# Kernel optimization log

Hardware: AMD Instinct MI355X
Metric: run time of the kernel (lower is better)

## Reference

```python
import jax, jax.numpy as jnp
import numpy as np

# dims: batch, fast time, fast/slow embed, heads, rate, ffn hidden, pool hidden, recombine hidden
B, T, D = 2, 2048, 512
H = 8
R = 8
DS = 512
FF = 2048
HP = 2048
HR = 2048


def _ln(x, g, b):
    m = jnp.mean(x, axis=-1, keepdims=True)
    v = jnp.var(x, axis=-1, keepdims=True)
    return (x - m) / jnp.sqrt(v + 1e-5) * g + b


def _encoder_layer(x, ln1_g, ln1_b, wqkv, bqkv, wo, bo, ln2_g, ln2_b, w1, b1, w2, b2, n_heads):
    # pre-LN transformer encoder layer with causal self-attention
    b_, t, d = x.shape
    dh = d // n_heads
    h = _ln(x, ln1_g, ln1_b)
    qkv = h @ wqkv + bqkv  # [B,T,3D]
    q, k, v = jnp.split(qkv, 3, axis=-1)
    q = q.reshape(b_, t, n_heads, dh)
    k = k.reshape(b_, t, n_heads, dh)
    v = v.reshape(b_, t, n_heads, dh)
    scores = jnp.einsum('bqhd,bkhd->bhqk', q, k) / jnp.sqrt(jnp.float32(dh))
    mask = jnp.tril(jnp.ones((t, t), dtype=bool))
    scores = jnp.where(mask, scores, jnp.finfo(scores.dtype).min)
    a = jax.nn.softmax(scores, axis=-1)
    o = jnp.einsum('bhqk,bkhd->bqhd', a, v).reshape(b_, t, d)
    x = x + o @ wo + bo
    h2 = _ln(x, ln2_g, ln2_b)
    return x + jax.nn.gelu(h2 @ w1 + b1) @ w2 + b2


def _pool(f, rate, wp1, bp1, wp2, bp2):
    # causal pooling: s_k = FFN(f_{k*rate : (k+1)*rate}), prepend zero step, drop last
    b_, t, d = f.shape
    k = t // rate
    xb = f[:, :k * rate].reshape(b_, k, rate * d)  # [B,K,rate*D] block flatten
    s = jax.nn.gelu(xb @ wp1 + bp1) @ wp2 + bp2  # [B,K,DS]
    s0 = jnp.zeros((b_, 1, s.shape[-1]), s.dtype)
    return jnp.concatenate([s0, s[:, :-1]], axis=1)


def _recombine(zf, zs, rate, wr1, br1, wr2, br2):
    # lift slow to fast scale (repeat_interleave along time), concat channels, 2-layer MLP
    zl = jnp.repeat(zs, rate, axis=1)[:, :zf.shape[1]]
    x = jnp.concatenate([zf, zl], axis=-1)
    return jax.nn.gelu(x @ wr1 + br1) @ wr2 + br2


def setup_inputs() -> dict:
    key = jax.random.key(0)
    ks = iter(jax.random.split(key, 64))

    def w(shape):
        return jax.random.normal(next(ks), shape, dtype=jnp.float32) * 0.02

    def z(shape):
        return jnp.zeros(shape, dtype=jnp.float32)

    def o(shape):
        return jnp.ones(shape, dtype=jnp.float32)

    inp = {'x': jax.random.normal(next(ks), (B, T, D), dtype=jnp.float32)}
    for suf, dm, ff in (('f', D, FF), ('s', DS, FF)):
        inp['ln1' + suf + '_g'] = o((dm,)); inp['ln1' + suf + '_b'] = z((dm,))
        inp['wqkv_' + suf] = w((dm, 3 * dm)); inp['bqkv_' + suf] = z((3 * dm,))
        inp['wo_' + suf] = w((dm, dm)); inp['bo_' + suf] = z((dm,))
        inp['ln2' + suf + '_g'] = o((dm,)); inp['ln2' + suf + '_b'] = z((dm,))
        inp['w1_' + suf] = w((dm, ff)); inp['b1_' + suf] = z((ff,))
        inp['w2_' + suf] = w((ff, dm)); inp['b2_' + suf] = z((dm,))
    inp['wp1'] = w((R * D, HP)); inp['bp1'] = z((HP,))
    inp['wp2'] = w((HP, DS)); inp['bp2'] = z((DS,))
    inp['wr1'] = w((D + DS, HR)); inp['br1'] = z((HR,))
    inp['wr2'] = w((HR, D)); inp['br2'] = z((D,))
    return inp


def reference(x, ln1f_g, ln1f_b, wqkv_f, bqkv_f, wo_f, bo_f, ln2f_g, ln2f_b, w1_f, b1_f, w2_f, b2_f,
              ln1s_g, ln1s_b, wqkv_s, bqkv_s, wo_s, bo_s, ln2s_g, ln2s_b, w1_s, b1_s, w2_s, b2_s,
              wp1, bp1, wp2, bp2, wr1, br1, wr2, br2):
    # fast-scale encoder layer
    zf = _encoder_layer(x, ln1f_g, ln1f_b, wqkv_f, bqkv_f, wo_f, bo_f,
                        ln2f_g, ln2f_b, w1_f, b1_f, w2_f, b2_f, H)
    # causal pool fast -> slow
    zs_in = _pool(zf, R, wp1, bp1, wp2, bp2)
    # slow-scale encoder layer
    zs = _encoder_layer(zs_in, ln1s_g, ln1s_b, wqkv_s, bqkv_s, wo_s, bo_s,
                        ln2s_g, ln2s_b, w1_s, b1_s, w2_s, b2_s, H)
    # lift + recombine back to fast scale
    return _recombine(zf, zs, R, wr1, br1, wr2, br2)
```

## Files before the change

kernel.cpp:

```cpp
#include <hip/hip_runtime.h>
#include <cstdint>

#define DEV __device__ __forceinline__

typedef float  floatx4 __attribute__((ext_vector_type(4)));
typedef __bf16 bf16x8  __attribute__((ext_vector_type(8)));
typedef short  short8  __attribute__((ext_vector_type(8)));

DEV unsigned short f2bf(float f) {
  unsigned u = __builtin_bit_cast(unsigned, f);
  u += 0x7FFFu + ((u >> 16) & 1u);
  return (unsigned short)(u >> 16);
}
DEV float bf2f(unsigned short s) {
  unsigned u = ((unsigned)s) << 16;
  return __builtin_bit_cast(float, u);
}
DEV float gelu_f(float x) {
  float x3 = x * x * x;
  return 0.5f * x * (1.0f + tanhf(0.7978845608028654f * (x + 0.044715f * x3)));
}

DEV void stage16(const unsigned short* g, unsigned short* l) {
  __builtin_amdgcn_global_load_lds(
      (const __attribute__((address_space(1))) void*)g,
      (__attribute__((address_space(3))) void*)l, 16, 0, 0);
}

struct TrArgs {
  const float* src[12];
  unsigned short* dst[12];
  int K[12];
  int N[12];
  int off[13];
};

__global__ __launch_bounds__(256) void transpose_all_k(TrArgs a) {
  __shared__ unsigned short tile[32][33];
  int bid = blockIdx.x;
  int w = 0;
#pragma unroll
  for (int i = 0; i < 11; ++i) if (bid >= a.off[i + 1]) w = i + 1;
  int loc = bid - a.off[w];
  int tn = a.N[w] >> 5;
  int nt = (loc % tn) * 32, kt = (loc / tn) * 32;
  const float* W = a.src[w];
  unsigned short* WT = a.dst[w];
  int K = a.K[w], N = a.N[w];

  int t = threadIdx.x;
  int rr = t >> 3, c4 = (t & 7) * 4;
  const float* src = W + (size_t)(kt + rr) * N + nt + c4;
  float4 v = *reinterpret_cast<const float4*>(src);
  tile[rr][c4 + 0] = f2bf(v.x); tile[rr][c4 + 1] = f2bf(v.y);
  tile[rr][c4 + 2] = f2bf(v.z); tile[rr][c4 + 3] = f2bf(v.w);
  __syncthreads();
  unsigned short* dst = WT + (size_t)(nt + rr) * K + kt + c4;
  ushort4 o;
  o.x = tile[c4 + 0][rr]; o.y = tile[c4 + 1][rr];
  o.z = tile[c4 + 2][rr]; o.w = tile[c4 + 3][rr];
  *reinterpret_cast<ushort4*>(dst) = o;
}

template <int NP, int ACT, int RES, int OBF>
__global__ __launch_bounds__(256) void reduceN_k(const float* __restrict__ part,
                                                 const float* __restrict__ bias,
                                                 const float* __restrict__ resid,
                                                 void* __restrict__ out,
                                                 int MN, int Nmask) {
  int i = (blockIdx.x * 256 + threadIdx.x) * 4;
  if (i >= MN) return;
  float4 v = *reinterpret_cast<const float4*>(&part[i]);
#pragma unroll
  for (int p = 1; p < NP; ++p) {
    float4 t = *reinterpret_cast<const float4*>(&part[(size_t)p * MN + i]);
    v.x += t.x; v.y += t.y; v.z += t.z; v.w += t.w;
  }
  float4 bv = *reinterpret_cast<const float4*>(&bias[i & Nmask]);
  v.x += bv.x; v.y += bv.y; v.z += bv.z; v.w += bv.w;
  if (RES) {
    float4 r = *reinterpret_cast<const float4*>(&resid[i]);
    v.x += r.x; v.y += r.y; v.z += r.z; v.w += r.w;
  }
  if (ACT) { v.x = gelu_f(v.x); v.y = gelu_f(v.y); v.z = gelu_f(v.z); v.w = gelu_f(v.w); }
  if (OBF) {
    ushort4 o; o.x = f2bf(v.x); o.y = f2bf(v.y); o.z = f2bf(v.z); o.w = f2bf(v.w);
    *reinterpret_cast<ushort4*>(&((unsigned short*)out)[i]) = o;
  } else {
    *reinterpret_cast<float4*>(&((float*)out)[i]) = v;
  }
}

__global__ __launch_bounds__(64) void ln_k(const float* __restrict__ in,
                                           const float* __restrict__ g,
                                           const float* __restrict__ be,
                                           unsigned short* __restrict__ out) {
  int row = blockIdx.x, lane = threadIdx.x;
  const float* p = in + (size_t)row * 512;
  float v[8], s = 0.f, sq = 0.f;
#pragma unroll
  for (int j = 0; j < 8; ++j) { v[j] = p[j * 64 + lane]; s += v[j]; sq += v[j] * v[j]; }
#pragma unroll
  for (int off = 32; off; off >>= 1) { s += __shfl_xor(s, off, 64); sq += __shfl_xor(sq, off, 64); }
  float mean = s * (1.f / 512.f);
  float var  = sq * (1.f / 512.f) - mean * mean;
  float rstd = rsqrtf(var + 1e-5f);
#pragma unroll
  for (int j = 0; j < 8; ++j) {
    int c = j * 64 + lane;
    out[(size_t)row * 512 + c] = f2bf((v[j] - mean) * rstd * g[c] + be[c]);
  }
}

__global__ __launch_bounds__(64) void rsln_k(const float* __restrict__ part,
                                             const float* __restrict__ bias,
                                             const float* __restrict__ g,
                                             const float* __restrict__ be,
                                             float* __restrict__ zsin,
                                             unsigned short* __restrict__ sh) {
  const int MN = 512 * 512;
  int j = blockIdx.x, lane = threadIdx.x;
  int k = j & 255;
  float v[8], s = 0.f, sq = 0.f;
  if (k == 0) {
#pragma unroll
    for (int jj = 0; jj < 8; ++jj) { v[jj] = 0.f; zsin[(size_t)j * 512 + jj * 64 + lane] = 0.f; }
  } else {
    const float* p = part + (size_t)(j - 1) * 512;
#pragma unroll
    for (int jj = 0; jj < 8; ++jj) {
      int c = jj * 64 + lane;
      float t = bias[c];
#pragma unroll
      for (int pp = 0; pp < 4; ++pp) t += p[(size_t)pp * MN + c];
      v[jj] = t;
      zsin[(size_t)j * 512 + c] = t;
      s += t; sq += t * t;
    }
  }
#pragma unroll
  for (int off = 32; off; off >>= 1) { s += __shfl_xor(s, off, 64); sq += __shfl_xor(sq, off, 64); }
  float mean = s * (1.f / 512.f);
  float var  = sq * (1.f / 512.f) - mean * mean;
  float rstd = rsqrtf(var + 1e-5f);
#pragma unroll
  for (int jj = 0; jj < 8; ++jj) {
    int c = jj * 64 + lane;
    sh[(size_t)j * 512 + c] = f2bf((v[jj] - mean) * rstd * g[c] + be[c]);
  }
}

template <int TM, int TN, int ACT, int RES, int OBF, int SPLITK, int CAT = 0>
__global__ __launch_bounds__(256) void gemm_k(const unsigned short* __restrict__ A,
                                              const unsigned short* __restrict__ A2,
                                              const unsigned short* __restrict__ WT,
                                              const float* __restrict__ bias,
                                              const float* __restrict__ resid,
                                              void* __restrict__ out,
                                              int M, int K, int N) {
  constexpr int WMn = (TN == 64) ? 2 : (TM / 64);
  constexpr int WNn = 4 / WMn;
  constexpr int MI  = TM / WMn / 16;
  constexpr int SN  = TN / WNn / 16;
  constexpr int APW = TM / 32;
  constexpr int BPW = TN / 32;
  __shared__ __align__(16) unsigned short As[2][TM * 64];
  __shared__ __align__(16) unsigned short Bs[2][TN * 64];
  const int tid  = threadIdx.x;
  const int wv = tid >> 6, lane = tid & 63;
  const int wm = wv / WNn, wn = wv % WNn;
  const int quad = lane >> 4, l16 = lane & 15;
  const int m0 = blockIdx.y * TM, n0 = blockIdx.x * TN;
  const int sp = (SPLITK > 1) ? blockIdx.z : 0;
  const int Kc = K / SPLITK;
  const int kb0 = sp * Kc;
  const int nk = Kc / 64;
  const int lrow = lane >> 3;
  const int scol = ((lane & 7) ^ lrow) * 8;
  const int sx = l16 & 7;

  floatx4 acc[MI][SN] = {};

  auto stage = [&](int buf, int kb) {
#pragma unroll
    for (int u = 0; u < APW; ++u) {
      int g = wv * APW + u;
      if (CAT) {
        int row = m0 + g * 8 + lrow;
        int kc = kb + scol;
        const unsigned short* s1 = A + (size_t)row * 512 + kc;
        const unsigned short* s2 = A2 +
            ((size_t)((row >> 11) * 256 + ((row & 2047) >> 3))) * 512 + (kc - 512);
        stage16(kc < 512 ? s1 : s2, &As[buf][g * 512]);
      } else {
        stage16(A + (size_t)(m0 + g * 8 + lrow) * K + kb + scol, &As[buf][g * 512]);
      }
    }
#pragma unroll
    for (int u = 0; u < BPW; ++u) {
      int g = wv * BPW + u;
      stage16(WT + (size_t)(n0 + g * 8 + lrow) * K + kb + scol, &Bs[buf][g * 512]);
    }
  };

  stage(0, kb0);
  __syncthreads();

  for (int t = 0; t < nk; ++t) {
    const int buf = t & 1;
    if (t + 1 < nk) stage(buf ^ 1, kb0 + (t + 1) * 64);
    bf16x8 af[MI][2], bfr[SN][2];
#pragma unroll
    for (int i = 0; i < MI; ++i) {
      const int r = wm * (MI * 16) + i * 16 + l16;
#pragma unroll
      for (int kk = 0; kk < 2; ++kk)
        af[i][kk] = *reinterpret_cast<const bf16x8*>(
            &As[buf][r * 64 + (((kk * 4 + quad) ^ sx) * 8)]);
    }
#pragma unroll
    for (int j = 0; j < SN; ++j) {
      const int r = wn * (SN * 16) + j * 16 + l16;
#pragma unroll
      for (int kk = 0; kk < 2; ++kk)
        bfr[j][kk] = *reinterpret_cast<const bf16x8*>(
            &Bs[buf][r * 64 + (((kk * 4 + quad) ^ sx) * 8)]);
    }
#pragma unroll
    for (int i = 0; i < MI; ++i)
#pragma unroll
      for (int j = 0; j < SN; ++j) {
        acc[i][j] = __builtin_amdgcn_mfma_f32_16x16x32_bf16(af[i][0], bfr[j][0], acc[i][j], 0, 0, 0);
        acc[i][j] = __builtin_amdgcn_mfma_f32_16x16x32_bf16(af[i][1], bfr[j][1], acc[i][j], 0, 0, 0);
      }
    __syncthreads();
  }

#pragma unroll
  for (int i = 0; i < MI; ++i) {
    int row_base = m0 + wm * (MI * 16) + i * 16 + quad * 4;
#pragma unroll
    for (int j = 0; j < SN; ++j) {
      int col = n0 + wn * (SN * 16) + j * 16 + l16;
      float bv = (SPLITK > 1) ? 0.f : bias[col];
#pragma unroll
      for (int rr = 0; rr < 4; ++rr) {
        int row = row_base + rr;
        float v = acc[i][j][rr];
        if (SPLITK > 1) {
          ((float*)out)[((size_t)sp * M + row) * N + col] = v;
        } else {
          v += bv;
          if (RES) v += resid[(size_t)row * N + col];
          if (ACT) v = gelu_f(v);
          if (OBF) ((unsigned short*)out)[(size_t)row * N + col] = f2bf(v);
          else     ((float*)out)[(size_t)row * N + col] = v;
        }
      }
    }
  }
}

__global__ __launch_bounds__(256) void attn_k(const unsigned short* __restrict__ qkv,
                                              unsigned short* __restrict__ out, int T) {
  const int ld = 1536, Dm = 512;
  __shared__ unsigned short Ks[2][64 * 72];
  __shared__ unsigned short Vt[2][64 * 72];
  __shared__ unsigned short ps[4][16 * 72];
  const int tid = threadIdx.x, wv = tid >> 6, lane = tid & 63;
  const int quad = lane >> 4, l16 = lane & 15;
  const int nqt = T >> 6;
  const int z = blockIdx.x;
  const int bh = z & 15;
  const int qt = nqt - 1 - (z >> 4);
  const int b = bh >> 3, hh = bh & 7;
  const int q0 = qt * 64 + wv * 16;
  const size_t bT = (size_t)b * T;

  const unsigned short* qp = qkv + (bT + q0 + l16) * ld + hh * 64 + quad * 8;
  short8 qa = *reinterpret_cast<const short8*>(qp);
  short8 qb = *reinterpret_cast<const short8*>(qp + 32);
  unsigned short qs0[8] __attribute__((aligned(16)));
  unsigned short qs1[8] __attribute__((aligned(16)));
#pragma unroll
  for (int u = 0; u < 8; ++u) {
    qs0[u] = f2bf(bf2f((unsigned short)qa[u]) * 0.125f);
    qs1[u] = f2bf(bf2f((unsigned short)qb[u]) * 0.125f);
  }
  bf16x8 aq0 = *reinterpret_cast<const bf16x8*>(qs0);
  bf16x8 aq1 = *reinterpret_cast<const bf16x8*>(qs1);

  floatx4 O[4] = {};
  float l_r[4] = {0.f, 0.f, 0.f, 0.f};

  const int nch = qt + 1;
  const int skey = tid >> 2, scc = (tid & 3) * 16;
  const int vkey = (tid & 31) * 2, vdg = tid >> 5;

  short8 kA, kB, vA, vB;
  auto prefetch = [&](int c) {
    const unsigned short* kp = qkv + (bT + c * 64 + skey) * ld + Dm + hh * 64 + scc;
    kA = *reinterpret_cast<const short8*>(kp);
    kB = *reinterpret_cast<const short8*>(kp + 8);
    const unsigned short* vp = qkv + (bT + c * 64 + vkey) * ld + 1024 + hh * 64 + vdg * 8;
    vA = *reinterpret_cast<const short8*>(vp);
    vB = *reinterpret_cast<const short8*>(vp + ld);
  };
  auto stage = [&](int buf) {
    *reinterpret_cast<short8*>(&Ks[buf][skey * 72 + scc])     = kA;
    *reinterpret_cast<short8*>(&Ks[buf][skey * 72 + scc + 8]) = kB;
#pragma unroll
    for (int u = 0; u < 8; ++u) {
      unsigned pk = ((unsigned)(unsigned short)vB[u] << 16) | (unsigned short)vA[u];
      *reinterpret_cast<unsigned*>(&Vt[buf][(vdg * 8 + u) * 72 + vkey]) = pk;
    }
  };

  prefetch(0);
  stage(0);
  __syncthreads();

  for (int c = 0; c < nch; ++c) {
    const int buf = c & 1;
    const bool last = (c == nch - 1);
    if (!last) prefetch(c + 1);

    floatx4 S[4];
    __builtin_amdgcn_s_setprio(1);
#pragma unroll
    for (int sub = 0; sub < 4; ++sub) {
      const unsigned short* kr = &Ks[buf][(sub * 16 + l16) * 72 + quad * 8];
      bf16x8 b0 = *reinterpret_cast<const bf16x8*>(kr);
      bf16x8 b1 = *reinterpret_cast<const bf16x8*>(kr + 32);
      floatx4 sacc = {};
      sacc = __builtin_amdgcn_mfma_f32_16x16x32_bf16(aq0, b0, sacc, 0, 0, 0);
      sacc = __builtin_amdgcn_mfma_f32_16x16x32_bf16(aq1, b1, sacc, 0, 0, 0);
      S[sub] = sacc;
    }
    __builtin_amdgcn_s_setprio(0);

    if (last) {
      const int k0 = c * 64;
#pragma unroll
      for (int r = 0; r < 4; ++r) {
        int qg = q0 + quad * 4 + r;
#pragma unroll
        for (int sub = 0; sub < 4; ++sub) {
          int kg = k0 + sub * 16 + l16;
          if (kg > qg) S[sub][r] = -3.0e38f;
        }
      }
    }
#pragma unroll
    for (int sub = 0; sub < 4; ++sub)
#pragma unroll
      for (int r = 0; r < 4; ++r) {
        float p = __expf(S[sub][r]);
        S[sub][r] = p;
        l_r[r] += p;
      }

#pragma unroll
    for (int sub = 0; sub < 4; ++sub)
#pragma unroll
      for (int r = 0; r < 4; ++r)
        ps[wv][(quad * 4 + r) * 72 + sub * 16 + l16] = f2bf(S[sub][r]);
    bf16x8 p0 = *reinterpret_cast<const bf16x8*>(&ps[wv][l16 * 72 + quad * 8]);
    bf16x8 p1 = *reinterpret_cast<const bf16x8*>(&ps[wv][l16 * 72 + 32 + quad * 8]);

    __builtin_amdgcn_s_setprio(1);
#pragma unroll
    for (int sd = 0; sd < 4; ++sd) {
      const unsigned short* vr = &Vt[buf][(sd * 16 + l16) * 72 + quad * 8];
      bf16x8 v0 = *reinterpret_cast<const bf16x8*>(vr);
      bf16x8 v1 = *reinterpret_cast<const bf16x8*>(vr + 32);
      O[sd] = __builtin_amdgcn_mfma_f32_16x16x32_bf16(p0, v0, O[sd], 0, 0, 0);
      O[sd] = __builtin_amdgcn_mfma_f32_16x16x32_bf16(p1, v1, O[sd], 0, 0, 0);
    }
    __builtin_amdgcn_s_setprio(0);

    if (!last) stage((c + 1) & 1);
    __syncthreads();
  }

#pragma unroll
  for (int r = 0; r < 4; ++r) {
    float l = l_r[r];
    l += __shfl_xor(l, 1, 64);
    l += __shfl_xor(l, 2, 64);
    l += __shfl_xor(l, 4, 64);
    l += __shfl_xor(l, 8, 64);
    l_r[r] = l;
  }

#pragma unroll
  for (int sd = 0; sd < 4; ++sd)
#pragma unroll
    for (int r = 0; r < 4; ++r) {
      int qg = q0 + quad * 4 + r;
      out[(bT + qg) * Dm + hh * 64 + sd * 16 + l16] = f2bf(O[sd][r] / l_r[r]);
    }
}

extern "C" void kernel_launch(void* const* d_in, const int* in_sizes, int n_in,
                              void* d_out, int out_size, void* d_ws, size_t ws_size,
                              hipStream_t stream) {
  (void)in_sizes; (void)n_in; (void)out_size; (void)ws_size;
  const int B = 2, T = 2048, FF = 2048, HP = 2048, HR = 2048;
  const int BT = B * T;
  const int BK = B * 256;

  const float* x      = (const float*)d_in[0];
  const float* ln1f_g = (const float*)d_in[1];
  const float* ln1f_b = (const float*)d_in[2];
  const float* wqkv_f = (const float*)d_in[3];
  const float* bqkv_f = (const float*)d_in[4];
  const float* wo_f   = (const float*)d_in[5];
  const float* bo_f   = (const float*)d_in[6];
  const float* ln2f_g = (const float*)d_in[7];
  const float* ln2f_b = (const float*)d_in[8];
  const float* w1_f   = (const float*)d_in[9];
  const float* b1_f   = (const float*)d_in[10];
  const float* w2_f   = (const float*)d_in[11];
  const float* b2_f   = (const float*)d_in[12];
  const float* ln1s_g = (const float*)d_in[13];
  const float* ln1s_b = (const float*)d_in[14];
  const float* wqkv_s = (const float*)d_in[15];
  const float* bqkv_s = (const float*)d_in[16];
  const float* wo_s   = (const float*)d_in[17];
  const float* bo_s   = (const float*)d_in[18];
  const float* ln2s_g = (const float*)d_in[19];
  const float* ln2s_b = (const float*)d_in[20];
  const float* w1_s   = (const float*)d_in[21];
  const float* b1_s   = (const float*)d_in[22];
  const float* w2_s   = (const float*)d_in[23];
  const float* b2_s   = (const float*)d_in[24];
  const float* wp1    = (const float*)d_in[25];
  const float* bp1    = (const float*)d_in[26];
  const float* wp2    = (const float*)d_in[27];
  const float* bp2    = (const float*)d_in[28];
  const float* wr1    = (const float*)d_in[29];
  const float* br1    = (const float*)d_in[30];
  const float* wr2    = (const float*)d_in[31];
  const float* br2    = (const float*)d_in[32];

  char* ws = (char*)d_ws;
  const size_t HMB = 512 * 1024;
  unsigned short* wtbase = (unsigned short*)(ws);
  unsigned short* h      = (unsigned short*)(ws + 76  * HMB);
  unsigned short* qkv    = (unsigned short*)(ws + 84  * HMB);
  unsigned short* attn   = (unsigned short*)(ws + 108 * HMB);
  float*          x1     = (float*)(ws + 116 * HMB);
  unsigned short* mid    = (unsigned short*)(ws + 132 * HMB);
  unsigned short* zf     = (unsigned short*)(ws + 164 * HMB);
  unsigned short* pmid   = (unsigned short*)(ws + 84  * HMB);
  float*          zsin   = (float*)(ws + 90  * HMB);
  unsigned short* sh     = (unsigned short*)(ws + 92  * HMB);
  unsigned short* sqkv   = (unsigned short*)(ws + 93  * HMB);
  unsigned short* sattn  = (unsigned short*)(ws + 96  * HMB);
  float*          sx1    = (float*)(ws + 97  * HMB);
  unsigned short* smid   = (unsigned short*)(ws + 99  * HMB);
  unsigned short* szs    = (unsigned short*)(ws + 103 * HMB);
  float*          part   = (float*)(ws + 172 * HMB);
  unsigned short* mid2   = (unsigned short*)(ws + 240 * HMB);

  size_t wo_off = 0;
  auto walloc = [&](size_t n) { unsigned short* p = wtbase + wo_off; wo_off += n; return p; };
  unsigned short* t_qkv_f = walloc((size_t)512 * 1536);
  unsigned short* t_wo_f  = walloc((size_t)512 * 512);
  unsigned short* t_w1_f  = walloc((size_t)512 * 2048);
  unsigned short* t_w2_f  = walloc((size_t)2048 * 512);
  unsigned short* t_qkv_s = walloc((size_t)512 * 1536);
  unsigned short* t_wo_s  = walloc((size_t)512 * 512);
  unsigned short* t_w1_s  = walloc((size_t)512 * 2048);
  unsigned short* t_w2_s  = walloc((size_t)2048 * 512);
  unsigned short* t_wp1   = walloc((size_t)4096 * 2048);
  unsigned short* t_wp2   = walloc((size_t)2048 * 512);
  unsigned short* t_wr1   = walloc((size_t)1024 * 2048);
  unsigned short* t_wr2   = walloc((size_t)2048 * 512);

  {
    TrArgs a;
    const float* srcs[12] = {wqkv_f, wo_f, w1_f, w2_f, wqkv_s, wo_s, w1_s, w2_s,
                             wp1, wp2, wr1, wr2};
    unsigned short* dsts[12] = {t_qkv_f, t_wo_f, t_w1_f, t_w2_f, t_qkv_s, t_wo_s,
                                t_w1_s, t_w2_s, t_wp1, t_wp2, t_wr1, t_wr2};
    int Ks[12] = {512, 512, 512, 2048, 512, 512, 512, 2048, 4096, 2048, 1024, 2048};
    int Ns[12] = {1536, 512, 2048, 512, 1536, 512, 2048, 512, 2048, 512, 2048, 512};
    int off = 0;
    for (int i = 0; i < 12; ++i) {
      a.src[i] = srcs[i]; a.dst[i] = dsts[i]; a.K[i] = Ks[i]; a.N[i] = Ns[i];
      a.off[i] = off;
      off += (Ks[i] / 32) * (Ns[i] / 32);
    }
    a.off[12] = off;
    transpose_all_k<<<off, 256, 0, stream>>>(a);
  }

  ln_k<<<BT, 64, 0, stream>>>(x, ln1f_g, ln1f_b, h);
  gemm_k<64, 128, 0, 0, 1, 1><<<dim3(12, 64), 256, 0, stream>>>(h, nullptr, t_qkv_f, bqkv_f, nullptr, qkv, BT, 512, 1536);
  attn_k<<<(T / 64) * 16, 256, 0, stream>>>(qkv, attn, T);
  gemm_k<64, 64, 0, 1, 0, 1><<<dim3(8, 64), 256, 0, stream>>>(attn, nullptr, t_wo_f, bo_f, x, x1, BT, 512, 512);
  ln_k<<<BT, 64, 0, stream>>>(x1, ln2f_g, ln2f_b, h);
  gemm_k<128, 128, 1, 0, 1, 1><<<dim3(16, 32), 256, 0, stream>>>(h, nullptr, t_w1_f, b1_f, nullptr, mid, BT, 512, FF);
  gemm_k<64, 64, 0, 1, 1, 1><<<dim3(8, 64), 256, 0, stream>>>(mid, nullptr, t_w2_f, b2_f, x1, zf, BT, FF, 512);

  gemm_k<128, 128, 0, 0, 0, 4><<<dim3(16, 4, 4), 256, 0, stream>>>(zf, nullptr, t_wp1, nullptr, nullptr, part, BK, 4096, HP);
  reduceN_k<4, 1, 0, 1><<<(BK * HP) / 1024, 256, 0, stream>>>(part, bp1, nullptr, pmid, BK * HP, HP - 1);
  gemm_k<64, 64, 0, 0, 0, 4><<<dim3(8, 8, 4), 256, 0, stream>>>(pmid, nullptr, t_wp2, nullptr, nullptr, part, BK, HP, 512);
  rsln_k<<<BK, 64, 0, stream>>>(part, bp2, ln1s_g, ln1s_b, zsin, sh);

  gemm_k<64, 64, 0, 0, 1, 1><<<dim3(24, 8), 256, 0, stream>>>(sh, nullptr, t_qkv_s, bqkv_s, nullptr, sqkv, BK, 512, 1536);
  attn_k<<<(256 / 64) * 16, 256, 0, stream>>>(sqkv, sattn, 256);
  gemm_k<64, 64, 0, 1, 0, 1><<<dim3(8, 8), 256, 0, stream>>>(sattn, nullptr, t_wo_s, bo_s, zsin, sx1, BK, 512, 512);
  ln_k<<<BK, 64, 0, stream>>>(sx1, ln2s_g, ln2s_b, sh);
  gemm_k<64, 64, 1, 0, 1, 1><<<dim3(32, 8), 256, 0, stream>>>(sh, nullptr, t_w1_s, b1_s, nullptr, smid, BK, 512, FF);
  gemm_k<64, 64, 0, 1, 1, 1><<<dim3(8, 8), 256, 0, stream>>>(smid, nullptr, t_w2_s, b2_s, sx1, szs, BK, FF, 512);

  gemm_k<128, 128, 1, 0, 1, 1, 1><<<dim3(16, 32), 256, 0, stream>>>(zf, szs, t_wr1, br1, nullptr, mid2, BT, 1024, HR);
  gemm_k<64, 64, 0, 0, 0, 1><<<dim3(8, 64), 256, 0, stream>>>(mid2, nullptr, t_wr2, br2, nullptr, d_out, BT, HR, 512);
}
```

Before: 429.8 us.

## Compute transposed attention scores to keep P in registers and load K directly

```diff
diff --git a/kernel.cpp b/kernel.cpp
--- a/kernel.cpp
+++ b/kernel.cpp
@@ -264,9 +264,7 @@
 __global__ __launch_bounds__(256) void attn_k(const unsigned short* __restrict__ qkv,
                                               unsigned short* __restrict__ out, int T) {
   const int ld = 1536, Dm = 512;
-  __shared__ unsigned short Ks[2][64 * 72];
   __shared__ unsigned short Vt[2][64 * 72];
-  __shared__ unsigned short ps[4][16 * 72];
   const int tid = threadIdx.x, wv = tid >> 6, lane = tid & 63;
   const int quad = lane >> 4, l16 = lane & 15;
   const int nqt = T >> 6;
@@ -291,24 +289,27 @@
   bf16x8 aq1 = *reinterpret_cast<const bf16x8*>(qs1);
 
   floatx4 O[4] = {};
-  float l_r[4] = {0.f, 0.f, 0.f, 0.f};
+  float l_sum = 0.f;
 
   const int nch = qt + 1;
-  const int skey = tid >> 2, scc = (tid & 3) * 16;
   const int vkey = (tid & 31) * 2, vdg = tid >> 5;
 
-  short8 kA, kB, vA, vB;
-  auto prefetch = [&](int c) {
-    const unsigned short* kp = qkv + (bT + c * 64 + skey) * ld + Dm + hh * 64 + scc;
-    kA = *reinterpret_cast<const short8*>(kp);
-    kB = *reinterpret_cast<const short8*>(kp + 8);
+  short8 kf[4][2];
+  auto loadK = [&](int c) {
+#pragma unroll
+    for (int sub = 0; sub < 4; ++sub) {
+      const unsigned short* kp = qkv + (bT + c * 64 + sub * 16 + l16) * ld + Dm + hh * 64 + quad * 8;
+      kf[sub][0] = *reinterpret_cast<const short8*>(kp);
+      kf[sub][1] = *reinterpret_cast<const short8*>(kp + 32);
+    }
+  };
+  short8 vA, vB;
+  auto prefetchV = [&](int c) {
     const unsigned short* vp = qkv + (bT + c * 64 + vkey) * ld + 1024 + hh * 64 + vdg * 8;
     vA = *reinterpret_cast<const short8*>(vp);
     vB = *reinterpret_cast<const short8*>(vp + ld);
   };
-  auto stage = [&](int buf) {
-    *reinterpret_cast<short8*>(&Ks[buf][skey * 72 + scc])     = kA;
-    *reinterpret_cast<short8*>(&Ks[buf][skey * 72 + scc + 8]) = kB;
+  auto stageV = [&](int buf) {
 #pragma unroll
     for (int u = 0; u < 8; ++u) {
       unsigned pk = ((unsigned)(unsigned short)vB[u] << 16) | (unsigned short)vA[u];
@@ -316,40 +317,40 @@
     }
   };
 
-  prefetch(0);
-  stage(0);
+  prefetchV(0);
+  loadK(0);
+  stageV(0);
   __syncthreads();
 
   for (int c = 0; c < nch; ++c) {
     const int buf = c & 1;
     const bool last = (c == nch - 1);
-    if (!last) prefetch(c + 1);
+    if (!last) prefetchV(c + 1);
 
     floatx4 S[4];
     __builtin_amdgcn_s_setprio(1);
 #pragma unroll
     for (int sub = 0; sub < 4; ++sub) {
-      const unsigned short* kr = &Ks[buf][(sub * 16 + l16) * 72 + quad * 8];
-      bf16x8 b0 = *reinterpret_cast<const bf16x8*>(kr);
-      bf16x8 b1 = *reinterpret_cast<const bf16x8*>(kr + 32);
       floatx4 sacc = {};
-      sacc = __builtin_amdgcn_mfma_f32_16x16x32_bf16(aq0, b0, sacc, 0, 0, 0);
-      sacc = __builtin_amdgcn_mfma_f32_16x16x32_bf16(aq1, b1, sacc, 0, 0, 0);
+      sacc = __builtin_amdgcn_mfma_f32_16x16x32_bf16(
+          __builtin_bit_cast(bf16x8, kf[sub][0]), aq0, sacc, 0, 0, 0);
+      sacc = __builtin_amdgcn_mfma_f32_16x16x32_bf16(
+          __builtin_bit_cast(bf16x8, kf[sub][1]), aq1, sacc, 0, 0, 0);
       S[sub] = sacc;
     }
     __builtin_amdgcn_s_setprio(0);
+    if (!last) loadK(c + 1);
 
     if (last) {
       const int k0 = c * 64;
-#pragma unroll
-      for (int r = 0; r < 4; ++r) {
-        int qg = q0 + quad * 4 + r;
-#pragma unroll
-        for (int sub = 0; sub < 4; ++sub) {
-          int kg = k0 + sub * 16 + l16;
+      const int qg = q0 + l16;
+#pragma unroll
+      for (int sub = 0; sub < 4; ++sub)
+#pragma unroll
+        for (int r = 0; r < 4; ++r) {
+          int kg = k0 + sub * 16 + quad * 4 + r;
           if (kg > qg) S[sub][r] = -3.0e38f;
         }
-      }
     }
 #pragma unroll
     for (int sub = 0; sub < 4; ++sub)
@@ -357,48 +358,55 @@
       for (int r = 0; r < 4; ++r) {
         float p = __expf(S[sub][r]);
         S[sub][r] = p;
-        l_r[r] += p;
+        l_sum += p;
       }
 
-#pragma unroll
-    for (int sub = 0; sub < 4; ++sub)
-#pragma unroll
-      for (int r = 0; r < 4; ++r)
-        ps[wv][(quad * 4 + r) * 72 + sub * 16 + l16] = f2bf(S[sub][r]);
-    bf16x8 p0 = *reinterpret_cast<const bf16x8*>(&ps[wv][l16 * 72 + quad * 8]);
-    bf16x8 p1 = *reinterpret_cast<const bf16x8*>(&ps[wv][l16 * 72 + 32 + quad * 8]);
+    short8 p0, p1;
+#pragma unroll
+    for (int j = 0; j < 4; ++j) {
+      p0[j]     = (short)f2bf(S[0][j]);
+      p0[4 + j] = (short)f2bf(S[1][j]);
+      p1[j]     = (short)f2bf(S[2][j]);
+      p1[4 + j] = (short)f2bf(S[3][j]);
+    }
+    bf16x8 pa0 = __builtin_bit_cast(bf16x8, p0);
+    bf16x8 pa1 = __builtin_bit_cast(bf16x8, p1);
 
     __builtin_amdgcn_s_setprio(1);
 #pragma unroll
     for (int sd = 0; sd < 4; ++sd) {
-      const unsigned short* vr = &Vt[buf][(sd * 16 + l16) * 72 + quad * 8];
-      bf16x8 v0 = *reinterpret_cast<const bf16x8*>(vr);
-      bf16x8 v1 = *reinterpret_cast<const bf16x8*>(vr + 32);
-      O[sd] = __builtin_amdgcn_mfma_f32_16x16x32_bf16(p0, v0, O[sd], 0, 0, 0);
-      O[sd] = __builtin_amdgcn_mfma_f32_16x16x32_bf16(p1, v1, O[sd], 0, 0, 0);
+      const unsigned short* vr = &Vt[buf][(sd * 16 + l16) * 72 + quad * 4];
+      short4 v0a = *reinterpret_cast<const short4*>(vr);
+      short4 v0b = *reinterpret_cast<const short4*>(vr + 16);
+      short4 v1a = *reinterpret_cast<const short4*>(vr + 32);
+      short4 v1b = *reinterpret_cast<const short4*>(vr + 48);
+      short8 w0, w1;
+      w0[0]=v0a.x; w0[1]=v0a.y; w0[2]=v0a.z; w0[3]=v0a.w;
+      w0[4]=v0b.x; w0[5]=v0b.y; w0[6]=v0b.z; w0[7]=v0b.w;
+      w1[0]=v1a.x; w1[1]=v1a.y; w1[2]=v1a.z; w1[3]=v1a.w;
+      w1[4]=v1b.x; w1[5]=v1b.y; w1[6]=v1b.z; w1[7]=v1b.w;
+      O[sd] = __builtin_amdgcn_mfma_f32_16x16x32_bf16(pa0, __builtin_bit_cast(bf16x8, w0), O[sd], 0, 0, 0);
+      O[sd] = __builtin_amdgcn_mfma_f32_16x16x32_bf16(pa1, __builtin_bit_cast(bf16x8, w1), O[sd], 0, 0, 0);
     }
     __builtin_amdgcn_s_setprio(0);
 
-    if (!last) stage((c + 1) & 1);
+    if (!last) stageV((c + 1) & 1);
     __syncthreads();
   }
 
-#pragma unroll
-  for (int r = 0; r < 4; ++r) {
-    float l = l_r[r];
-    l += __shfl_xor(l, 1, 64);
-    l += __shfl_xor(l, 2, 64);
-    l += __shfl_xor(l, 4, 64);
-    l += __shfl_xor(l, 8, 64);
-    l_r[r] = l;
-  }
+  l_sum += __shfl_xor(l_sum, 16, 64);
+  l_sum += __shfl_xor(l_sum, 32, 64);
+  float lq[4];
+#pragma unroll
+  for (int r = 0; r < 4; ++r)
+    lq[r] = __shfl(l_sum, quad * 4 + r, 64);
 
 #pragma unroll
   for (int sd = 0; sd < 4; ++sd)
 #pragma unroll
     for (int r = 0; r < 4; ++r) {
       int qg = q0 + quad * 4 + r;
-      out[(bT + qg) * Dm + hh * 64 + sd * 16 + l16] = f2bf(O[sd][r] / l_r[r]);
+      out[(bT + qg) * Dm + hh * 64 + sd * 16 + l16] = f2bf(O[sd][r] / lq[r]);
     }
 }
 
```

Measured after the change: 448.2 us. 1.04x slower.
